# Kernel optimization log

Measured on AMD Instinct MI355X. Metric: run time of the kernel, lower is better.

The kernel has to match this reference:

```python
import jax, jax.numpy as jnp
import numpy as np

BLOCK = 32  # GGUF Q8_0 block size: one scale per 32 int8 quants


def setup_inputs() -> dict:
    key = jax.random.key(0)
    k1, k2, k3, k4 = jax.random.split(key, 4)
    B, S, D_IN, D_OUT = 2, 2048, 4096, 16384
    x = jax.random.normal(k1, (B, S, D_IN), dtype=jnp.float32)
    # Stored quantized weights: unsigned byte codes in [0,255]; dequant as (q-128)*scale
    weight_q = jax.random.randint(k2, (D_OUT, D_IN), 0, 255, dtype=jnp.int32)
    # One positive scale per 32-element block along in_features
    scales = jax.random.uniform(k3, (D_OUT, D_IN // BLOCK), dtype=jnp.float32) * 0.02 + 1e-3
    bias = jax.random.normal(k4, (D_OUT,), dtype=jnp.float32)
    return {"x": x, "weight_q": weight_q, "scales": scales, "bias": bias}


def _dequant(weight_q, scales):
    # weight_q: [O, I] int codes, scales: [O, I/BLOCK] -> fp weight [O, I]
    O, I = weight_q.shape
    q = (weight_q.astype(jnp.float32) - 128.0).reshape(O, I // BLOCK, BLOCK)
    return (q * scales[:, :, None]).reshape(O, I)


def reference(x, weight_q, scales, bias):
    # Fused dequant + matmul: y = x @ dequant(W).T + bias
    w = _dequant(weight_q, scales)  # [O, I]
    y = jnp.einsum("bsi,oi->bso", x, w)
    return y + bias
```

## Files before the change

kernel.cpp:

```cpp
#include <hip/hip_runtime.h>
#include <hip/hip_bf16.h>

typedef __attribute__((ext_vector_type(8))) short short8;
typedef __attribute__((ext_vector_type(4))) float f32x4;

#define AS1 __attribute__((address_space(1)))
#define AS3 __attribute__((address_space(3)))

static __device__ __forceinline__ short f2bf(float f) {
    __hip_bfloat16 h = __float2bfloat16(f);
    union { __hip_bfloat16 h; short s; } u;
    u.h = h;
    return u.s;
}


__global__ __launch_bounds__(256) void prepack_w_kernel(const int* __restrict__ wq,
                                                        const float* __restrict__ scales,
                                                        short* __restrict__ Wb,
                                                        long total8) {
    long i = (long)blockIdx.x * 256 + threadIdx.x;
    if (i >= total8) return;
    const int4* p = (const int4*)wq + i * 2;
    int4 q0 = p[0], q1 = p[1];
    float s = scales[(i * 8) >> 5];
    short8 v;
    v[0] = f2bf((float)(q0.x - 128) * s);
    v[1] = f2bf((float)(q0.y - 128) * s);
    v[2] = f2bf((float)(q0.z - 128) * s);
    v[3] = f2bf((float)(q0.w - 128) * s);
    v[4] = f2bf((float)(q1.x - 128) * s);
    v[5] = f2bf((float)(q1.y - 128) * s);
    v[6] = f2bf((float)(q1.z - 128) * s);
    v[7] = f2bf((float)(q1.w - 128) * s);
    ((short8*)Wb)[i] = v;
}

__global__ __launch_bounds__(256) void prepack_x_kernel(const float* __restrict__ x,
                                                        short* __restrict__ Xb,
                                                        long total8) {
    long i = (long)blockIdx.x * 256 + threadIdx.x;
    if (i >= total8) return;
    const float4* p = (const float4*)x + i * 2;
    float4 f0 = p[0], f1 = p[1];
    short8 v;
    v[0] = f2bf(f0.x); v[1] = f2bf(f0.y); v[2] = f2bf(f0.z); v[3] = f2bf(f0.w);
    v[4] = f2bf(f1.x); v[5] = f2bf(f1.y); v[6] = f2bf(f1.z); v[7] = f2bf(f1.w);
    ((short8*)Xb)[i] = v;
}

__global__ __launch_bounds__(512, 2)
void gemm256_kernel(const float* __restrict__ bias,
                    const short* __restrict__ Xb, const short* __restrict__ Wb,
                    float* __restrict__ out, int M, int N, int K) {
    __shared__ alignas(16) short As[4 * 8192];
    __shared__ alignas(16) short Bs[4 * 8192];

    const int nM = M >> 8, nN = N >> 8;
    int bid = blockIdx.x;
    {
        int nwg = nM * nN;
        if ((nwg & 7) == 0) bid = (bid & 7) * (nwg >> 3) + (bid >> 3);
    }
    int pm, pn;
    {
        const int G = 8;
        if ((nN % G) == 0) {
            int per = nM * G;
            int grp = bid / per, in = bid % per;
            pn = grp * G + (in % G);
            pm = in / G;
        } else { pn = bid % nN; pm = bid / nN; }
    }

    const int tid  = threadIdx.x;
    const int lane = tid & 63;
    const int wid  = tid >> 6;
    const int wm   = wid >> 2;
    const int wn   = wid & 3;
    const int q4   = lane >> 4;
    const int l15  = lane & 15;
    const int lx   = lane & 7;

    const long bm = (long)pm << 8, bn = (long)pn << 8;
    const long Kl = K;
    const int  NT = K >> 6;

    const int rA0 = wm * 8192 + l15 * 64;
    const int rA1 = (2 + wm) * 8192 + l15 * 64;
    const int rB0 = (wn >> 1) * 8192 + ((wn & 1) * 64 + l15) * 64;
    const int rB1 = (2 + (wn >> 1)) * 8192 + ((wn & 1) * 64 + l15) * 64;
    const int sg0 = (q4 ^ lx) * 8;
    const int sg1 = ((4 + q4) ^ lx) * 8;

    const int chnk    = wid * 1024;
    const int srowrel = wid * 16 + (lane >> 3);
    const int scol    = ((lane & 7) ^ (lane >> 3)) * 8;

    const short* aS00 = Xb + (bm + 0   + srowrel + 0) * Kl + scol;
    const short* aS01 = Xb + (bm + 0   + srowrel + 8) * Kl + scol;
    const short* aS10 = Xb + (bm + 128 + srowrel + 0) * Kl + scol;
    const short* aS11 = Xb + (bm + 128 + srowrel + 8) * Kl + scol;
    const short* bS00 = Wb + (bn + 0   + srowrel + 0) * Kl + scol;
    const short* bS01 = Wb + (bn + 0   + srowrel + 8) * Kl + scol;
    const short* bS10 = Wb + (bn + 128 + srowrel + 0) * Kl + scol;
    const short* bS11 = Wb + (bn + 128 + srowrel + 8) * Kl + scol;

#define STGA(H, PARL, OFF) {                                                          \
    __builtin_amdgcn_global_load_lds((const AS1 void*)(aS##H##0 + (OFF)),             \
        (AS3 void*)&As[((PARL) * 2 + (H)) * 8192 + chnk], 16, 0, 0);                  \
    __builtin_amdgcn_global_load_lds((const AS1 void*)(aS##H##1 + (OFF)),             \
        (AS3 void*)&As[((PARL) * 2 + (H)) * 8192 + chnk + 512], 16, 0, 0); }
#define STGB(H, PARL, OFF) {                                                          \
    __builtin_amdgcn_global_load_lds((const AS1 void*)(bS##H##0 + (OFF)),             \
        (AS3 void*)&Bs[((PARL) * 2 + (H)) * 8192 + chnk], 16, 0, 0);                  \
    __builtin_amdgcn_global_load_lds((const AS1 void*)(bS##H##1 + (OFF)),             \
        (AS3 void*)&Bs[((PARL) * 2 + (H)) * 8192 + chnk + 512], 16, 0, 0); }

#define QUAD(Q, RA) {                                                                 \
    ak[0][0] = *(const short8*)&As[(RA) + (2 * (Q)) * 1024 + sg0];                    \
    ak[0][1] = *(const short8*)&As[(RA) + (2 * (Q)) * 1024 + sg1];                    \
    ak[1][0] = *(const short8*)&As[(RA) + (2 * (Q) + 1) * 1024 + sg0];                \
    ak[1][1] = *(const short8*)&As[(RA) + (2 * (Q) + 1) * 1024 + sg1]; }
#define LDB8(RB) { _Pragma("unroll") for (int n = 0; n < 4; ++n) {                    \
    bfr[n][0] = *(const short8*)&Bs[(RB) + n * 1024 + sg0];                           \
    bfr[n][1] = *(const short8*)&Bs[(RB) + n * 1024 + sg1]; } }

#define MFMA16(Q) { __builtin_amdgcn_s_setprio(1);                                    \
    _Pragma("unroll") for (int mi = 0; mi < 2; ++mi) {                                \
        _Pragma("unroll") for (int n = 0; n < 4; ++n)                                 \
            acc[2 * (Q) + mi][n] = __builtin_amdgcn_mfma_f32_16x16x32_bf16(           \
                ak[mi][0], bfr[n][0], acc[2 * (Q) + mi][n], 0, 0, 0);                 \
        _Pragma("unroll") for (int n = 0; n < 4; ++n)                                 \
            acc[2 * (Q) + mi][n] = __builtin_amdgcn_mfma_f32_16x16x32_bf16(           \
                ak[mi][1], bfr[n][1], acc[2 * (Q) + mi][n], 0, 0, 0); }               \
    __builtin_amdgcn_s_setprio(0); }

#define BAR  __builtin_amdgcn_s_barrier()
#define WLG0 { asm volatile("s_waitcnt lgkmcnt(0)" ::: "memory");                     \
               __builtin_amdgcn_sched_barrier(0); }
#define WLG8 asm volatile("s_waitcnt lgkmcnt(8)" ::: "memory")

    f32x4 acc[8][4];
#pragma unroll
    for (int m = 0; m < 8; ++m)
#pragma unroll
        for (int n = 0; n < 4; ++n) acc[m][n] = (f32x4){0.f, 0.f, 0.f, 0.f};

    short8 ak[2][2], bfr[4][2];

    STGB(0, 0, 0); STGB(1, 0, 0);
    STGA(0, 0, 0); STGA(1, 0, 0);
    STGB(0, 1, 64); STGB(1, 1, 64);
    asm volatile("s_waitcnt vmcnt(4)" ::: "memory");
    BAR;

    for (int t = 0; t + 3 < NT; t += 2) {
        const long o1 = ((long)t + 1) << 6;
        const long o2 = o1 + 64;
        const long o3 = o2 + 64;
        QUAD(0, rA0); LDB8(rB0); STGA(0, 1, o1); WLG8; BAR; WLG0; MFMA16(0); BAR;
        QUAD(1, rA0); STGA(1, 1, o1); BAR; WLG0; MFMA16(1); BAR;
        QUAD(2, rA0); STGB(0, 0, o2); BAR; WLG0; MFMA16(2); BAR;
        QUAD(3, rA0); STGB(1, 0, o2); BAR; WLG0; MFMA16(3);
        asm volatile("s_waitcnt vmcnt(4)" ::: "memory"); BAR;
        QUAD(0, rA1); LDB8(rB1); STGA(0, 0, o2); WLG8; BAR; WLG0; MFMA16(0); BAR;
        QUAD(1, rA1); STGA(1, 0, o2); BAR; WLG0; MFMA16(1); BAR;
        QUAD(2, rA1); STGB(0, 1, o3); BAR; WLG0; MFMA16(2); BAR;
        QUAD(3, rA1); STGB(1, 1, o3); BAR; WLG0; MFMA16(3);
        asm volatile("s_waitcnt vmcnt(4)" ::: "memory"); BAR;
    }

    {
        const long o1 = ((long)NT - 1) << 6;
        QUAD(0, rA0); LDB8(rB0); STGA(0, 1, o1); WLG8; BAR; WLG0; MFMA16(0); BAR;
        QUAD(1, rA0); STGA(1, 1, o1); BAR; WLG0; MFMA16(1); BAR;
        QUAD(2, rA0); BAR; WLG0; MFMA16(2); BAR;
        QUAD(3, rA0); BAR; WLG0; MFMA16(3);
        asm volatile("s_waitcnt vmcnt(0)" ::: "memory"); BAR;
        QUAD(0, rA1); LDB8(rB1); WLG8; BAR; WLG0; MFMA16(0); BAR;
        QUAD(1, rA1); BAR; WLG0; MFMA16(1); BAR;
        QUAD(2, rA1); BAR; WLG0; MFMA16(2); BAR;
        QUAD(3, rA1); WLG0; MFMA16(3);
    }

#pragma unroll
    for (int n = 0; n < 4; ++n) {
        long col = bn + wn * 64 + n * 16 + l15;
        float bv = bias[col];
#pragma unroll
        for (int m = 0; m < 8; ++m) {
            long row = bm + wm * 128 + m * 16 + q4 * 4;
#pragma unroll
            for (int r = 0; r < 4; ++r)
                out[(row + r) * (long)N + col] = acc[m][n][r] + bv;
        }
    }
#undef STGA
#undef STGB
#undef QUAD
#undef LDB8
#undef MFMA16
#undef BAR
#undef WLG0
#undef WLG8
}


template <bool PRE_A, bool PRE_B>
__global__ __launch_bounds__(256, 2)
void gemm_kernel(const float* __restrict__ x, const int* __restrict__ wq,
                 const float* __restrict__ scales, const float* __restrict__ bias,
                 const short* __restrict__ Xb, const short* __restrict__ Wb,
                 float* __restrict__ out, int M, int N, int K) {
    constexpr int BM = 128, BN = 128, BK = 64;
    __shared__ alignas(16) short As[BM * BK];
    __shared__ alignas(16) short Bs[BN * BK];

    const int nM = M / BM, nN = N / BN;
    int bid = blockIdx.x;
    int pm, pn;
    const int G = 8;
    if ((nN % G) == 0) {
        int per = nM * G;
        int grp = bid / per;
        int in  = bid % per;
        pn = grp * G + (in % G);
        pm = in / G;
    } else {
        pn = bid % nN;
        pm = bid / nN;
    }

    const int tid  = threadIdx.x;
    const int lane = tid & 63;
    const int wv   = tid >> 6;
    const int wm   = (wv >> 1) * 64;
    const int wn   = (wv & 1) * 64;
    const int q    = lane >> 4;
    const int l15  = lane & 15;
    const int sxor = lane & 7;

    const long bm = (long)pm * BM, bn = (long)pn * BN;

    f32x4 acc[4][4];
#pragma unroll
    for (int i = 0; i < 4; ++i)
#pragma unroll
        for (int j = 0; j < 4; ++j) acc[i][j] = (f32x4){0.f, 0.f, 0.f, 0.f};

    const int srow = tid >> 3;
    const int scg  = tid & 7;

    const int sg0   = q ^ sxor;
    const int aOff0 = (wm + l15) * 64 + sg0 * 8;
    const int aOff1 = (wm + l15) * 64 + (sg0 ^ 4) * 8;
    const int bOff0 = (wn + l15) * 64 + sg0 * 8;
    const int bOff1 = (wn + l15) * 64 + (sg0 ^ 4) * 8;

    const int prRow  = lane >> 3;
    const int prGsrc = (lane & 7) ^ (lane >> 3);

    for (int k0 = 0; k0 < K; k0 += BK) {
        if constexpr (PRE_A) {
#pragma unroll
            for (int i = 0; i < 4; ++i) {
                int r = wv * 32 + i * 8 + prRow;
                const short* src = Xb + (bm + r) * (long)K + k0 + prGsrc * 8;
                __builtin_amdgcn_global_load_lds((const AS1 void*)src,
                                                 (AS3 void*)&As[(wv * 32 + i * 8) * 64],
                                                 16, 0, 0);
            }
        } else {
#pragma unroll
            for (int i = 0; i < 4; ++i) {
                int r = i * 32 + srow;
                const float4* p = (const float4*)(x + (bm + r) * (long)K + k0 + scg * 8);
                float4 f0 = p[0], f1 = p[1];
                short8 v;
                v[0] = f2bf(f0.x); v[1] = f2bf(f0.y); v[2] = f2bf(f0.z); v[3] = f2bf(f0.w);
                v[4] = f2bf(f1.x); v[5] = f2bf(f1.y); v[6] = f2bf(f1.z); v[7] = f2bf(f1.w);
                int sg = scg ^ (r & 7);
                *(short8*)&As[r * 64 + sg * 8] = v;
            }
        }
        if constexpr (PRE_B) {
#pragma unroll
            for (int i = 0; i < 4; ++i) {
                int r = wv * 32 + i * 8 + prRow;
                const short* src = Wb + (bn + r) * (long)K + k0 + prGsrc * 8;
                __builtin_amdgcn_global_load_lds((const AS1 void*)src,
                                                 (AS3 void*)&Bs[(wv * 32 + i * 8) * 64],
                                                 16, 0, 0);
            }
        } else {
#pragma unroll
            for (int i = 0; i < 4; ++i) {
                int r = i * 32 + srow;
                const int4* p = (const int4*)(wq + (bn + r) * (long)K + k0 + scg * 8);
                int4 q0 = p[0], q1 = p[1];
                float s = scales[(bn + r) * (long)(K >> 5) + ((k0 + scg * 8) >> 5)];
                short8 v;
                v[0] = f2bf((float)(q0.x - 128) * s);
                v[1] = f2bf((float)(q0.y - 128) * s);
                v[2] = f2bf((float)(q0.z - 128) * s);
                v[3] = f2bf((float)(q0.w - 128) * s);
                v[4] = f2bf((float)(q1.x - 128) * s);
                v[5] = f2bf((float)(q1.y - 128) * s);
                v[6] = f2bf((float)(q1.z - 128) * s);
                v[7] = f2bf((float)(q1.w - 128) * s);
                int sg = scg ^ (r & 7);
                *(short8*)&Bs[r * 64 + sg * 8] = v;
            }
        }
        __syncthreads();

#pragma unroll
        for (int kk = 0; kk < 2; ++kk) {
            short8 a[4], b[4];
            const int aBase = kk ? aOff1 : aOff0;
            const int bBase = kk ? bOff1 : bOff0;
#pragma unroll
            for (int mi = 0; mi < 4; ++mi) a[mi] = *(const short8*)&As[aBase + mi * 16 * 64];
#pragma unroll
            for (int nj = 0; nj < 4; ++nj) b[nj] = *(const short8*)&Bs[bBase + nj * 16 * 64];
#pragma unroll
            for (int mi = 0; mi < 4; ++mi)
#pragma unroll
                for (int nj = 0; nj < 4; ++nj)
                    acc[mi][nj] = __builtin_amdgcn_mfma_f32_16x16x32_bf16(
                        a[mi], b[nj], acc[mi][nj], 0, 0, 0);
        }
        __syncthreads();
    }

#pragma unroll
    for (int nj = 0; nj < 4; ++nj) {
        long col = bn + wn + nj * 16 + l15;
        float bv = bias[col];
#pragma unroll
        for (int mi = 0; mi < 4; ++mi) {
            long row = bm + wm + mi * 16 + q * 4;
#pragma unroll
            for (int r2 = 0; r2 < 4; ++r2)
                out[(row + r2) * (long)N + col] = acc[mi][nj][r2] + bv;
        }
    }
}


extern "C" void kernel_launch(void* const* d_in, const int* in_sizes, int n_in,
                              void* d_out, int out_size, void* d_ws, size_t ws_size,
                              hipStream_t stream) {
    const float* x      = (const float*)d_in[0];
    const int*   wq     = (const int*)d_in[1];
    const float* scales = (const float*)d_in[2];
    const float* bias   = (const float*)d_in[3];
    float*       out    = (float*)d_out;

    const long N = (long)in_sizes[3];
    const long K = (long)in_sizes[1] / N;
    const long M = (long)in_sizes[0] / K;

    const size_t needW = (size_t)N * K * sizeof(short);
    const size_t needX = (size_t)M * K * sizeof(short);

    short* Wb = (short*)d_ws;
    short* Xb = Wb + (size_t)N * K;

    const bool preB = (d_ws != nullptr) && ws_size >= needW;
    const bool preA = preB && ws_size >= (needW + needX);

    if (preB) {
        long t8 = N * K / 8;
        prepack_w_kernel<<<dim3((unsigned)((t8 + 255) / 256)), dim3(256), 0, stream>>>(
            wq, scales, Wb, t8);
    }
    if (preA) {
        long t8 = M * K / 8;
        prepack_x_kernel<<<dim3((unsigned)((t8 + 255) / 256)), dim3(256), 0, stream>>>(
            x, Xb, t8);
    }

    const long NTl = K / 64;
    const bool big = preA && (M % 256 == 0) && (N % 256 == 0) && (K % 64 == 0) &&
                     (NTl >= 2) && (NTl % 2 == 0);

    if (big) {
        dim3 grid((unsigned)((M / 256) * (N / 256))), block(512);
        gemm256_kernel<<<grid, block, 0, stream>>>(bias, Xb, Wb, out, (int)M, (int)N, (int)K);
    } else {
        dim3 grid((unsigned)((M / 128) * (N / 128))), block(256);
        if (preA)
            gemm_kernel<true, true><<<grid, block, 0, stream>>>(x, wq, scales, bias, Xb, Wb,
                                                                out, (int)M, (int)N, (int)K);
        else if (preB)
            gemm_kernel<false, true><<<grid, block, 0, stream>>>(x, wq, scales, bias, Xb, Wb,
                                                                 out, (int)M, (int)N, (int)K);
        else
            gemm_kernel<false, false><<<grid, block, 0, stream>>>(x, wq, scales, bias, Xb, Wb,
                                                                  out, (int)M, (int)N, (int)K);
    }
}
```

Before: 605.5 us.

## Double-buffer LDS fragment registers to overlap ds_reads with MFMA in 256 GEMM

Splits the A and B fragment registers into ping-pong buffers so the LDS reads for the next quarter-step are issued before the MFMAs of the current one. Waits become partial lgkmcnt counts instead of draining to zero, and the B fragments for the next K-tile are prefetched one phase early. This aims to hide LDS read latency behind matrix-core work, at the cost of more VGPRs and a more intricate wait and barrier schedule. The minimum K-tile count for the big path rises to 4 to fit the deeper prologue.

```diff
diff --git a/kernel.cpp b/kernel.cpp
--- a/kernel.cpp
+++ b/kernel.cpp
@@ -117,29 +117,29 @@
     __builtin_amdgcn_global_load_lds((const AS1 void*)(bS##H##1 + (OFF)),             \
         (AS3 void*)&Bs[((PARL) * 2 + (H)) * 8192 + chnk + 512], 16, 0, 0); }
 
-#define QUAD(Q, RA) {                                                                 \
-    ak[0][0] = *(const short8*)&As[(RA) + (2 * (Q)) * 1024 + sg0];                    \
-    ak[0][1] = *(const short8*)&As[(RA) + (2 * (Q)) * 1024 + sg1];                    \
-    ak[1][0] = *(const short8*)&As[(RA) + (2 * (Q) + 1) * 1024 + sg0];                \
-    ak[1][1] = *(const short8*)&As[(RA) + (2 * (Q) + 1) * 1024 + sg1]; }
-#define LDB8(RB) { _Pragma("unroll") for (int n = 0; n < 4; ++n) {                    \
-    bfr[n][0] = *(const short8*)&Bs[(RB) + n * 1024 + sg0];                           \
-    bfr[n][1] = *(const short8*)&Bs[(RB) + n * 1024 + sg1]; } }
-
-#define MFMA16(Q) { __builtin_amdgcn_s_setprio(1);                                    \
+#define QUAD(Q, RA, BUF) {                                                            \
+    BUF[0][0] = *(const short8*)&As[(RA) + (2 * (Q)) * 1024 + sg0];                   \
+    BUF[0][1] = *(const short8*)&As[(RA) + (2 * (Q)) * 1024 + sg1];                   \
+    BUF[1][0] = *(const short8*)&As[(RA) + (2 * (Q) + 1) * 1024 + sg0];               \
+    BUF[1][1] = *(const short8*)&As[(RA) + (2 * (Q) + 1) * 1024 + sg1]; }
+#define LDB8(RB, BUF) { _Pragma("unroll") for (int n = 0; n < 4; ++n) {               \
+    BUF[n][0] = *(const short8*)&Bs[(RB) + n * 1024 + sg0];                           \
+    BUF[n][1] = *(const short8*)&Bs[(RB) + n * 1024 + sg1]; } }
+
+#define MFMA16(Q, A, B) { __builtin_amdgcn_s_setprio(1);                              \
     _Pragma("unroll") for (int mi = 0; mi < 2; ++mi) {                                \
         _Pragma("unroll") for (int n = 0; n < 4; ++n)                                 \
             acc[2 * (Q) + mi][n] = __builtin_amdgcn_mfma_f32_16x16x32_bf16(           \
-                ak[mi][0], bfr[n][0], acc[2 * (Q) + mi][n], 0, 0, 0);                 \
+                A[mi][0], B[n][0], acc[2 * (Q) + mi][n], 0, 0, 0);                    \
         _Pragma("unroll") for (int n = 0; n < 4; ++n)                                 \
             acc[2 * (Q) + mi][n] = __builtin_amdgcn_mfma_f32_16x16x32_bf16(           \
-                ak[mi][1], bfr[n][1], acc[2 * (Q) + mi][n], 0, 0, 0); }               \
+                A[mi][1], B[n][1], acc[2 * (Q) + mi][n], 0, 0, 0); }                  \
     __builtin_amdgcn_s_setprio(0); }
 
 #define BAR  __builtin_amdgcn_s_barrier()
-#define WLG0 { asm volatile("s_waitcnt lgkmcnt(0)" ::: "memory");                     \
-               __builtin_amdgcn_sched_barrier(0); }
-#define WLG8 asm volatile("s_waitcnt lgkmcnt(8)" ::: "memory")
+#define WLGN(n) { asm volatile("s_waitcnt lgkmcnt(" #n ")" ::: "memory");             \
+                  __builtin_amdgcn_sched_barrier(0); }
+#define VMC(n)  asm volatile("s_waitcnt vmcnt(" #n ")" ::: "memory")
 
     f32x4 acc[8][4];
 #pragma unroll
@@ -147,41 +147,43 @@
 #pragma unroll
         for (int n = 0; n < 4; ++n) acc[m][n] = (f32x4){0.f, 0.f, 0.f, 0.f};
 
-    short8 ak[2][2], bfr[4][2];
+    short8 akA[2][2], akB[2][2], bfP[4][2], bfN[4][2];
 
     STGB(0, 0, 0); STGB(1, 0, 0);
     STGA(0, 0, 0); STGA(1, 0, 0);
     STGB(0, 1, 64); STGB(1, 1, 64);
-    asm volatile("s_waitcnt vmcnt(4)" ::: "memory");
+    VMC(4);
     BAR;
+    LDB8(rB0, bfP); QUAD(0, rA0, akA);
 
     for (int t = 0; t + 3 < NT; t += 2) {
         const long o1 = ((long)t + 1) << 6;
         const long o2 = o1 + 64;
         const long o3 = o2 + 64;
-        QUAD(0, rA0); LDB8(rB0); STGA(0, 1, o1); WLG8; BAR; WLG0; MFMA16(0); BAR;
-        QUAD(1, rA0); STGA(1, 1, o1); BAR; WLG0; MFMA16(1); BAR;
-        QUAD(2, rA0); STGB(0, 0, o2); BAR; WLG0; MFMA16(2); BAR;
-        QUAD(3, rA0); STGB(1, 0, o2); BAR; WLG0; MFMA16(3);
-        asm volatile("s_waitcnt vmcnt(4)" ::: "memory"); BAR;
-        QUAD(0, rA1); LDB8(rB1); STGA(0, 0, o2); WLG8; BAR; WLG0; MFMA16(0); BAR;
-        QUAD(1, rA1); STGA(1, 0, o2); BAR; WLG0; MFMA16(1); BAR;
-        QUAD(2, rA1); STGB(0, 1, o3); BAR; WLG0; MFMA16(2); BAR;
-        QUAD(3, rA1); STGB(1, 1, o3); BAR; WLG0; MFMA16(3);
-        asm volatile("s_waitcnt vmcnt(4)" ::: "memory"); BAR;
+        QUAD(1, rA0, akB); STGA(0, 1, o1); BAR; WLGN(4); MFMA16(0, akA, bfP); BAR;
+        QUAD(2, rA0, akA); STGA(1, 1, o1); BAR; WLGN(4); MFMA16(1, akB, bfP); BAR;
+        QUAD(3, rA0, akB); STGB(0, 0, o2); BAR; WLGN(4); MFMA16(2, akA, bfP);
+        VMC(2); BAR;
+        LDB8(rB1, bfN); QUAD(0, rA1, akA); STGB(1, 0, o2); BAR; WLGN(12);
+        MFMA16(3, akB, bfP); BAR;
+        QUAD(1, rA1, akB); STGA(0, 0, o2); BAR; WLGN(4); MFMA16(0, akA, bfN); BAR;
+        QUAD(2, rA1, akA); STGA(1, 0, o2); BAR; WLGN(4); MFMA16(1, akB, bfN); BAR;
+        QUAD(3, rA1, akB); STGB(0, 1, o3); BAR; WLGN(4); MFMA16(2, akA, bfN);
+        VMC(2); BAR;
+        LDB8(rB0, bfP); QUAD(0, rA0, akA); STGB(1, 1, o3); BAR; WLGN(12);
+        MFMA16(3, akB, bfN); BAR;
     }
 
     {
         const long o1 = ((long)NT - 1) << 6;
-        QUAD(0, rA0); LDB8(rB0); STGA(0, 1, o1); WLG8; BAR; WLG0; MFMA16(0); BAR;
-        QUAD(1, rA0); STGA(1, 1, o1); BAR; WLG0; MFMA16(1); BAR;
-        QUAD(2, rA0); BAR; WLG0; MFMA16(2); BAR;
-        QUAD(3, rA0); BAR; WLG0; MFMA16(3);
-        asm volatile("s_waitcnt vmcnt(0)" ::: "memory"); BAR;
-        QUAD(0, rA1); LDB8(rB1); WLG8; BAR; WLG0; MFMA16(0); BAR;
-        QUAD(1, rA1); BAR; WLG0; MFMA16(1); BAR;
-        QUAD(2, rA1); BAR; WLG0; MFMA16(2); BAR;
-        QUAD(3, rA1); WLG0; MFMA16(3);
+        QUAD(1, rA0, akB); STGA(0, 1, o1); BAR; WLGN(4); MFMA16(0, akA, bfP); BAR;
+        QUAD(2, rA0, akA); STGA(1, 1, o1); BAR; WLGN(4); MFMA16(1, akB, bfP); BAR;
+        QUAD(3, rA0, akB); BAR; WLGN(4); MFMA16(2, akA, bfP); VMC(0); BAR;
+        LDB8(rB1, bfN); QUAD(0, rA1, akA); BAR; WLGN(12); MFMA16(3, akB, bfP); BAR;
+        QUAD(1, rA1, akB); BAR; WLGN(4); MFMA16(0, akA, bfN); BAR;
+        QUAD(2, rA1, akA); BAR; WLGN(4); MFMA16(1, akB, bfN); BAR;
+        QUAD(3, rA1, akB); BAR; WLGN(4); MFMA16(2, akA, bfN); BAR;
+        WLGN(0); MFMA16(3, akB, bfN);
     }
 
 #pragma unroll
@@ -202,8 +204,8 @@
 #undef LDB8
 #undef MFMA16
 #undef BAR
-#undef WLG0
-#undef WLG8
+#undef WLGN
+#undef VMC
 }
 
 
@@ -384,7 +386,7 @@
 
     const long NTl = K / 64;
     const bool big = preA && (M % 256 == 0) && (N % 256 == 0) && (K % 64 == 0) &&
-                     (NTl >= 2) && (NTl % 2 == 0);
+                     (NTl >= 4) && (NTl % 2 == 0);
 
     if (big) {
         dim3 grid((unsigned)((M / 256) * (N / 256))), block(512);
```

Result: slower. 1.071 ms (+76.9%).
